# Kernel optimization log

Hardware: AMD Instinct MI355X
Metric: run time of the kernel (lower is better)

Reference implementation:

```python
import jax, jax.numpy as jnp
import numpy as np

B, T, D = 2, 4096, 512
H = 8
HD = D // H


def setup_inputs() -> dict:
    key = jax.random.key(0)
    ks = jax.random.split(key, 6)
    s = 0.02
    return {
        "token_embed": jax.random.normal(ks[0], (B, T, D), jnp.float32),
        "Wq": jax.random.normal(ks[1], (D, D), jnp.float32) * s,
        "Wk": jax.random.normal(ks[2], (D, D), jnp.float32) * s,
        "Wv": jax.random.normal(ks[3], (D, D), jnp.float32) * s,
        "Wo": jax.random.normal(ks[4], (D, D), jnp.float32) * s,
        "bo": jnp.zeros((D,), jnp.float32),
    }


def reference(token_embed, Wq, Wk, Wv, Wo, bo):
    b, t, d_in = token_embed.shape
    # QKV projections (Linear without bias): x @ W^T with W stored [d_out, d_in]
    q = jnp.einsum("btd,ed->bte", token_embed, Wq).reshape(b, t, H, HD).transpose(0, 2, 1, 3)
    k = jnp.einsum("btd,ed->bte", token_embed, Wk).reshape(b, t, H, HD).transpose(0, 2, 1, 3)
    v = jnp.einsum("btd,ed->bte", token_embed, Wv).reshape(b, t, H, HD).transpose(0, 2, 1, 3)
    # Scores [b, h, t, t] with causal mask applied before scaling (as in source)
    scores = jnp.einsum("bhqd,bhkd->bhqk", q, k)
    causal = jnp.tril(jnp.ones((t, t), bool))  # True = keep
    scores = jnp.where(causal, scores, -jnp.inf)
    attn = jax.nn.softmax(scores / jnp.sqrt(jnp.float32(HD)), axis=-1)
    # dropout p=0.0 -> identity
    ctx = jnp.einsum("bhqk,bhkd->bhqd", attn, v)
    ctx = ctx.transpose(0, 2, 1, 3).reshape(b, t, H * HD)
    return jnp.einsum("btd,ed->bte", ctx, Wo) + bo
```

## Files before the change

kernel.cpp:

```cpp
#include <hip/hip_runtime.h>

#define B_  2
#define T_  4096
#define D_  512
#define H_  8
#define HD_ 64
#define M_  (B_*T_)

typedef _Float16 h16;
typedef _Float16 v8h __attribute__((ext_vector_type(8)));
typedef float v4f __attribute__((ext_vector_type(4)));
typedef unsigned short us;

#define AS1 __attribute__((address_space(1)))
#define AS3 __attribute__((address_space(3)))

__device__ __forceinline__ float bf2f(us u){
  union { unsigned int i; float f; } v; v.i = ((unsigned int)u) << 16; return v.f;
}
__device__ __forceinline__ us f2bf(float f){
  union { float f; unsigned int u; } v; v.f = f;
  unsigned int r = v.u + 0x7FFFu + ((v.u >> 16) & 1u);
  return (us)(r >> 16);
}
__device__ __forceinline__ v4f zero4(){ v4f z; z[0]=0.f; z[1]=0.f; z[2]=0.f; z[3]=0.f; return z; }

__device__ __forceinline__ void glds16(const h16* g, h16* l){
  __builtin_amdgcn_global_load_lds((const AS1 int*)(const void*)g,
                                   (AS3 int*)(void*)l, 16, 0, 0);
}

__global__ __launch_bounds__(256) void conv_all(
    const void* __restrict__ x, const void* __restrict__ w0, const void* __restrict__ w1,
    const void* __restrict__ w2, const void* __restrict__ w3, const void* __restrict__ bo,
    h16* __restrict__ xb, h16* __restrict__ d0, h16* __restrict__ d1,
    h16* __restrict__ d2, h16* __restrict__ d3, float* __restrict__ bof)
{
  const int bid = blockIdx.x, tid = threadIdx.x;
  const void* src; int o0; int seg;
  h16* dst = nullptr;
  if (bid < 16384)      { src = x; o0 = bid * 256; dst = xb; seg = 0; }
  else if (bid < 20480) {
    const int wsel = (bid - 16384) >> 10;
    src = (wsel == 0) ? w0 : (wsel == 1) ? w1 : (wsel == 2) ? w2 : w3;
    dst = (wsel == 0) ? d0 : (wsel == 1) ? d1 : (wsel == 2) ? d2 : d3;
    o0 = ((bid - 16384) & 1023) * 256; seg = 0;
  } else                { src = bo; o0 = (bid - 20480) * 256; seg = 1; }

  __shared__ int sflag;
  if (tid == 0) sflag = 0;
  __syncthreads();
  const float probe = bf2f(((const us*)src)[o0 + tid]);
  if (!(fabsf(probe) < 1e4f)) atomicAdd(&sflag, 1);
  __syncthreads();
  const int isf32 = (sflag != 0);
  const int i = o0 + tid;
  const float v = isf32 ? ((const float*)src)[i] : bf2f(((const us*)src)[i]);
  if (seg) bof[i] = v;
  else     dst[i] = (h16)v;
}

__device__ __forceinline__ void stage4(const h16* __restrict__ A, const h16* __restrict__ W,
                                       int m0, int n0, int kk, h16* sA, h16* sB, int tid){
  const int colA = (tid & 3) << 3;
  const int rowT = tid >> 2;
#pragma unroll
  for (int rd = 0; rd < 2; rd++) {
    const int row = rd * 64 + rowT;
    const int f = rd * 2048 + tid * 8;
    glds16(A + (size_t)(m0 + row) * D_ + kk + colA, sA + f);
    glds16(W + (size_t)(n0 + row) * D_ + kk + colA, sB + f);
  }
}

__device__ __forceinline__ void gemm_core(const h16* __restrict__ A,
                                          const h16* __restrict__ W,
                                          int m0, int n0, h16* sA, h16* sB,
                                          v4f acc[4][4]) {
  const int tid = threadIdx.x;
  const int lane = tid & 63, wid = tid >> 6;
  const int r = lane & 15, q = lane >> 4;
#pragma unroll
  for (int i = 0; i < 4; i++)
#pragma unroll
    for (int j = 0; j < 4; j++) acc[i][j] = zero4();

  stage4(A, W, m0, n0, 0, sA, sB, tid);
#pragma unroll 1
  for (int kt = 0; kt < 16; kt++) {
    if (kt < 15) {
      const int nb = (kt + 1) & 1;
      stage4(A, W, m0, n0, (kt + 1) * 32, sA + nb * 4096, sB + nb * 4096, tid);
      asm volatile("s_waitcnt vmcnt(4)" ::: "memory");
    } else {
      asm volatile("s_waitcnt vmcnt(0)" ::: "memory");
    }
    asm volatile("s_barrier" ::: "memory");
    const h16* pA = sA + (kt & 1) * 4096 + ((wid & 1) * 64 + r) * 32 + q * 8;
    const h16* pB = sB + (kt & 1) * 4096 + ((wid >> 1) * 64 + r) * 32 + q * 8;
    v8h a[4], b[4];
#pragma unroll
    for (int i = 0; i < 4; i++) a[i] = *(const v8h*)(pA + i * 512);
#pragma unroll
    for (int j = 0; j < 4; j++) b[j] = *(const v8h*)(pB + j * 512);
#pragma unroll
    for (int i = 0; i < 4; i++)
#pragma unroll
      for (int j = 0; j < 4; j++)
        acc[i][j] = __builtin_amdgcn_mfma_f32_16x16x32_f16(a[i], b[j], acc[i][j], 0, 0, 0);
    asm volatile("s_barrier" ::: "memory");
  }
}

__global__ __launch_bounds__(256, 3) void gemm_qkv(
    const h16* __restrict__ X,
    const h16* __restrict__ Wq, const h16* __restrict__ Wk, const h16* __restrict__ Wv,
    h16* __restrict__ Qo, h16* __restrict__ Ko, h16* __restrict__ VTo)
{
  __shared__ h16 sA[2 * 4096], sB[2 * 4096];
  const h16* W = (blockIdx.z == 0) ? Wq : (blockIdx.z == 1 ? Wk : Wv);
  const int m0 = blockIdx.x * 128, n0 = blockIdx.y * 128;
  v4f acc[4][4];
  gemm_core(X, W, m0, n0, sA, sB, acc);
  const int lane = threadIdx.x & 63, wid = threadIdx.x >> 6;
  const int r = lane & 15, q = lane >> 4;
  const int wm = m0 + (wid & 1) * 64, wn = n0 + (wid >> 1) * 64;
  if (blockIdx.z == 2) {
#pragma unroll
    for (int i = 0; i < 4; i++)
#pragma unroll
      for (int j = 0; j < 4; j++)
#pragma unroll
        for (int rr = 0; rr < 4; rr++) {
          const int row = wm + i*16 + q*4 + rr;
          const int col = wn + j*16 + r;
          const int bb = row >> 12, tt = row & (T_ - 1);
          const int hh = col >> 6,  hd = col & 63;
          const int t6 = tt & 63;
          const int tperm = (tt & ~63) | (t6 & 3) | (((t6 >> 2) & 3) << 3)
                          | (((t6 >> 4) & 1) << 2) | (t6 & 32);
          VTo[((size_t)(((bb << 3) + hh) << 6) + hd) * T_ + tperm] = (h16)acc[i][j][rr];
        }
  } else {
    h16* Y = (blockIdx.z == 0) ? Qo : Ko;
    const float sc = (blockIdx.z == 0) ? 0.1803368801f : 1.0f;
#pragma unroll
    for (int i = 0; i < 4; i++)
#pragma unroll
      for (int j = 0; j < 4; j++)
#pragma unroll
        for (int rr = 0; rr < 4; rr++)
          Y[(size_t)(wm + i*16 + q*4 + rr) * D_ + wn + j*16 + r] = (h16)(acc[i][j][rr] * sc);
  }
}

__global__ __launch_bounds__(256, 3) void gemm_out(
    const h16* __restrict__ A, const h16* __restrict__ W,
    const float* __restrict__ bias, void* __restrict__ out, const void* __restrict__ xprobe)
{
  __shared__ h16 sA[2 * 4096], sB[2 * 4096];
  __shared__ int sflag;
  if (threadIdx.x == 0) sflag = 0;
  __syncthreads();
  const float probe = bf2f(((const us*)xprobe)[threadIdx.x]);
  if (!(fabsf(probe) < 1e4f)) atomicAdd(&sflag, 1);
  __syncthreads();
  const int flag = (sflag != 0);

  const int m0 = blockIdx.x * 128, n0 = blockIdx.y * 128;
  v4f acc[4][4];
  gemm_core(A, W, m0, n0, sA, sB, acc);
  const int lane = threadIdx.x & 63, wid = threadIdx.x >> 6;
  const int r = lane & 15, q = lane >> 4;
  const int wm = m0 + (wid & 1) * 64, wn = n0 + (wid >> 1) * 64;
#pragma unroll
  for (int i = 0; i < 4; i++)
#pragma unroll
    for (int j = 0; j < 4; j++)
#pragma unroll
      for (int rr = 0; rr < 4; rr++) {
        const int row = wm + i*16 + q*4 + rr;
        const int col = wn + j*16 + r;
        const float v = acc[i][j][rr] + bias[col];
        if (flag) ((float*)out)[(size_t)row * D_ + col] = v;
        else ((us*)out)[(size_t)row * D_ + col] = f2bf(v);
      }
}

__global__ __launch_bounds__(256, 4) void attn_kernel(
    const h16* __restrict__ Q, const h16* __restrict__ K,
    const h16* __restrict__ VT, h16* __restrict__ Ctx)
{
  const int h = blockIdx.x;
  const int pos = blockIdx.y + (blockIdx.z << 6);
  const int qc = 63 - (pos >> 1);
  const int b  = pos & 1;
  const int tid = threadIdx.x;
  const int wid = tid >> 6, lane = tid & 63;
  const int r = lane & 15, quad = lane >> 4;

  const size_t headoff = (size_t)b * T_ * D_ + (size_t)h * HD_;
  const h16* Qh  = Q + headoff;
  const h16* Kh  = K + headoff;
  const h16* VTh = VT + (size_t)(b * H_ + h) * HD_ * T_;
  h16* Ch = Ctx + headoff;

  __shared__ h16 sK[2][4096];
  __shared__ h16 sV[2][4096];

  const int qrow = qc * 64 + wid * 16;
  const int ntiles = qc + 1;

  const v8h aq0 = *(const v8h*)(Qh + (size_t)(qrow + r) * D_ + quad * 8);
  const v8h aq1 = *(const v8h*)(Qh + (size_t)(qrow + r) * D_ + 32 + quad * 8);

  v4f o[4];
#pragma unroll
  for (int j = 0; j < 4; j++) o[j] = zero4();
  float lsum = 0.f;

#pragma unroll
  for (int p = 0; p < 2; p++) {
    const int u = p * 256 + tid;
    const int row = u >> 3, j = u & 7, gj = j ^ (row & 7);
    glds16(Kh + (size_t)row * D_ + gj * 8, &sK[0][u * 8]);
  }
#pragma unroll
  for (int p = 0; p < 2; p++) {
    const int u = p * 256 + tid;
    const int row = u >> 3, j = u & 7, gj = j ^ (row & 7);
    glds16(VTh + (size_t)row * T_ + gj * 8, &sV[0][u * 8]);
  }

#pragma unroll 1
  for (int kt = 0; kt < ntiles; kt++) {
    const h16* sKc = sK[kt & 1];
    const h16* sVc = sV[kt & 1];
    if (kt + 1 < ntiles) {
      const int nb = (kt + 1) & 1;
      const int kb1 = (kt + 1) << 6;
#pragma unroll
      for (int p = 0; p < 2; p++) {
        const int u = p * 256 + tid;
        const int row = u >> 3, j = u & 7, gj = j ^ (row & 7);
        glds16(Kh + (size_t)(kb1 + row) * D_ + gj * 8, &sK[nb][u * 8]);
      }
#pragma unroll
      for (int p = 0; p < 2; p++) {
        const int u = p * 256 + tid;
        const int row = u >> 3, j = u & 7, gj = j ^ (row & 7);
        glds16(VTh + (size_t)row * T_ + kb1 + gj * 8, &sV[nb][u * 8]);
      }
      asm volatile("s_waitcnt vmcnt(4)" ::: "memory");
    } else {
      asm volatile("s_waitcnt vmcnt(0)" ::: "memory");
    }
    asm volatile("s_barrier" ::: "memory");

    const int kb = kt << 6;
    v8h ka[8], va[8];
#pragma unroll
    for (int kf = 0; kf < 4; kf++) {
      const int rowk = kf * 16 + r;
      const h16* base = sKc + rowk * 64;
      ka[2*kf]   = *(const v8h*)(base + ((quad     ^ (rowk & 7)) * 8));
      ka[2*kf+1] = *(const v8h*)(base + (((quad+4) ^ (rowk & 7)) * 8));
    }
#pragma unroll
    for (int j = 0; j < 4; j++) {
      const int rowv = j * 16 + r;
      const h16* base = sVc + rowv * 64;
      va[2*j]   = *(const v8h*)(base + ((quad     ^ (rowv & 7)) * 8));
      va[2*j+1] = *(const v8h*)(base + (((quad+4) ^ (rowv & 7)) * 8));
    }
    v4f s[4];
#pragma unroll
    for (int i = 0; i < 4; i++) {
      v4f t = zero4();
      t = __builtin_amdgcn_mfma_f32_16x16x32_f16(ka[2*i],   aq0, t, 0, 0, 0);
      t = __builtin_amdgcn_mfma_f32_16x16x32_f16(ka[2*i+1], aq1, t, 0, 0, 0);
      s[i] = t;
    }
    const bool maskt = (kt == ntiles - 1);
    v8h pa0, pa1;
#pragma unroll
    for (int i = 0; i < 4; i++) {
#pragma unroll
      for (int rr = 0; rr < 4; rr++) {
        float scv = s[i][rr];
        if (maskt) scv = (kb + i * 16 + quad * 4 + rr <= qrow + r) ? scv : -1e30f;
        const float e = exp2f(scv);
        lsum += e;
        if (i < 2) pa0[i * 4 + rr] = (h16)e;
        else       pa1[(i - 2) * 4 + rr] = (h16)e;
      }
    }
#pragma unroll
    for (int j = 0; j < 4; j++) {
      o[j] = __builtin_amdgcn_mfma_f32_16x16x32_f16(pa0, va[2*j],   o[j], 0, 0, 0);
      o[j] = __builtin_amdgcn_mfma_f32_16x16x32_f16(pa1, va[2*j+1], o[j], 0, 0, 0);
    }
    asm volatile("s_barrier" ::: "memory");
  }
  float l = lsum;
  l += __shfl_xor(l, 16, 64);
  l += __shfl_xor(l, 32, 64);
  const float inv = 1.0f / l;
  float invr[4];
#pragma unroll
  for (int rr = 0; rr < 4; rr++) invr[rr] = __shfl(inv, quad * 4 + rr, 16);
#pragma unroll
  for (int rr = 0; rr < 4; rr++) {
    const size_t row = (size_t)(qrow + quad * 4 + rr) * D_;
#pragma unroll
    for (int j = 0; j < 4; j++)
      Ch[row + j * 16 + r] = (h16)(o[j][rr] * invr[rr]);
  }
}

extern "C" void kernel_launch(void* const* d_in, const int* in_sizes, int n_in,
                              void* d_out, int out_size, void* d_ws, size_t ws_size,
                              hipStream_t stream) {
  char* ws = (char*)d_ws;
  h16* xb  = (h16*)(ws + 0);
  h16* qb  = (h16*)(ws + 8388608);
  h16* kb  = (h16*)(ws + 16777216);
  h16* vt  = (h16*)(ws + 25165824);
  h16* ctx = (h16*)(ws + 33554432);
  h16* wqb = (h16*)(ws + 41943040);
  h16* wkb = (h16*)(ws + 41943040 + 524288);
  h16* wvb = (h16*)(ws + 41943040 + 2 * 524288);
  h16* wob = (h16*)(ws + 41943040 + 3 * 524288);
  float* bof = (float*)(ws + 41943040 + 4 * 524288);

  conv_all<<<20482, 256, 0, stream>>>(d_in[0], d_in[1], d_in[2], d_in[3], d_in[4],
                                      d_in[5], xb, wqb, wkb, wvb, wob, bof);
  gemm_qkv<<<dim3(M_ / 128, D_ / 128, 3), 256, 0, stream>>>(xb, wqb, wkb, wvb, qb, kb, vt);
  attn_kernel<<<dim3(H_, 64, B_), 256, 0, stream>>>(qb, kb, vt, ctx);
  gemm_out<<<dim3(M_ / 128, D_ / 128, 1), 256, 0, stream>>>(ctx, wob, bof, d_out, d_in[0]);
}
```

Measured before the change: 196.8 us.

## Process two 64-row query groups per attention block to reuse K/V tiles

Each attention block now handles 128 query rows, as two 64-row groups, instead of 64, so every K/V tile loaded into shared memory serves both groups. This roughly halves global K/V traffic and barrier overhead per query row. Blocks are scheduled in a heavy/light interleaved order to balance causal work, and shared-memory pointer arithmetic is simplified with incrementing pointers. The grid is halved and launch bounds are relaxed to allow more registers, which risks lower occupancy and fewer blocks to fill the device.

```diff
diff --git a/kernel.cpp b/kernel.cpp
--- a/kernel.cpp
+++ b/kernel.cpp
@@ -187,14 +187,14 @@
       }
 }
 
-__global__ __launch_bounds__(256, 4) void attn_kernel(
+__global__ __launch_bounds__(256, 2) void attn_kernel(
     const h16* __restrict__ Q, const h16* __restrict__ K,
     const h16* __restrict__ VT, h16* __restrict__ Ctx)
 {
   const int h = blockIdx.x;
-  const int pos = blockIdx.y + (blockIdx.z << 6);
-  const int qc = 63 - (pos >> 1);
-  const int b  = pos & 1;
+  const int s = blockIdx.y + (blockIdx.z << 5);
+  const int qc = (s < 32) ? (31 - (s >> 1)) : ((s - 32) >> 1);
+  const int b  = s & 1;
   const int tid = threadIdx.x;
   const int wid = tid >> 6, lane = tid & 63;
   const int r = lane & 15, quad = lane >> 4;
@@ -208,29 +208,34 @@
   __shared__ h16 sK[2][4096];
   __shared__ h16 sV[2][4096];
 
-  const int qrow = qc * 64 + wid * 16;
-  const int ntiles = qc + 1;
-
-  const v8h aq0 = *(const v8h*)(Qh + (size_t)(qrow + r) * D_ + quad * 8);
-  const v8h aq1 = *(const v8h*)(Qh + (size_t)(qrow + r) * D_ + 32 + quad * 8);
-
-  v4f o[4];
-#pragma unroll
-  for (int j = 0; j < 4; j++) o[j] = zero4();
-  float lsum = 0.f;
-
-#pragma unroll
-  for (int p = 0; p < 2; p++) {
-    const int u = p * 256 + tid;
-    const int row = u >> 3, j = u & 7, gj = j ^ (row & 7);
-    glds16(Kh + (size_t)row * D_ + gj * 8, &sK[0][u * 8]);
-  }
-#pragma unroll
-  for (int p = 0; p < 2; p++) {
-    const int u = p * 256 + tid;
-    const int row = u >> 3, j = u & 7, gj = j ^ (row & 7);
-    glds16(VTh + (size_t)row * T_ + gj * 8, &sV[0][u * 8]);
-  }
+  const int qg0 = qc * 128 + wid * 16;
+  const int qg1 = qg0 + 64;
+  const int ntiles = 2 * qc + 2;
+  const int diag0 = 2 * qc, diag1 = 2 * qc + 1;
+
+  const v8h aq00 = *(const v8h*)(Qh + (size_t)(qg0 + r) * D_ + quad * 8);
+  const v8h aq01 = *(const v8h*)(Qh + (size_t)(qg0 + r) * D_ + 32 + quad * 8);
+  const v8h aq10 = *(const v8h*)(Qh + (size_t)(qg1 + r) * D_ + quad * 8);
+  const v8h aq11 = *(const v8h*)(Qh + (size_t)(qg1 + r) * D_ + 32 + quad * 8);
+
+  v4f o0[4], o1[4];
+#pragma unroll
+  for (int j = 0; j < 4; j++) { o0[j] = zero4(); o1[j] = zero4(); }
+  float lsum0 = 0.f, lsum1 = 0.f;
+
+  const int u0 = tid, u1 = tid + 256;
+  const int sr0 = u0 >> 3, sj0 = (u0 & 7) ^ (sr0 & 7);
+  const int sr1 = u1 >> 3, sj1 = (u1 & 7) ^ (sr1 & 7);
+  const h16* kp0 = Kh + (size_t)sr0 * D_ + sj0 * 8;
+  const h16* kp1 = Kh + (size_t)sr1 * D_ + sj1 * 8;
+  const h16* vp0 = VTh + (size_t)sr0 * T_ + sj0 * 8;
+  const h16* vp1 = VTh + (size_t)sr1 * T_ + sj1 * 8;
+
+  glds16(kp0, &sK[0][u0 * 8]);
+  glds16(kp1, &sK[0][u1 * 8]);
+  glds16(vp0, &sV[0][u0 * 8]);
+  glds16(vp1, &sV[0][u1 * 8]);
+  kp0 += 64 * D_; kp1 += 64 * D_; vp0 += 64; vp1 += 64;
 
 #pragma unroll 1
   for (int kt = 0; kt < ntiles; kt++) {
@@ -238,83 +243,89 @@
     const h16* sVc = sV[kt & 1];
     if (kt + 1 < ntiles) {
       const int nb = (kt + 1) & 1;
-      const int kb1 = (kt + 1) << 6;
-#pragma unroll
-      for (int p = 0; p < 2; p++) {
-        const int u = p * 256 + tid;
-        const int row = u >> 3, j = u & 7, gj = j ^ (row & 7);
-        glds16(Kh + (size_t)(kb1 + row) * D_ + gj * 8, &sK[nb][u * 8]);
-      }
-#pragma unroll
-      for (int p = 0; p < 2; p++) {
-        const int u = p * 256 + tid;
-        const int row = u >> 3, j = u & 7, gj = j ^ (row & 7);
-        glds16(VTh + (size_t)row * T_ + kb1 + gj * 8, &sV[nb][u * 8]);
-      }
+      glds16(kp0, &sK[nb][u0 * 8]);
+      glds16(kp1, &sK[nb][u1 * 8]);
+      glds16(vp0, &sV[nb][u0 * 8]);
+      glds16(vp1, &sV[nb][u1 * 8]);
+      kp0 += 64 * D_; kp1 += 64 * D_; vp0 += 64; vp1 += 64;
       asm volatile("s_waitcnt vmcnt(4)" ::: "memory");
     } else {
       asm volatile("s_waitcnt vmcnt(0)" ::: "memory");
     }
     asm volatile("s_barrier" ::: "memory");
 
-    const int kb = kt << 6;
     v8h ka[8], va[8];
 #pragma unroll
     for (int kf = 0; kf < 4; kf++) {
       const int rowk = kf * 16 + r;
       const h16* base = sKc + rowk * 64;
-      ka[2*kf]   = *(const v8h*)(base + ((quad     ^ (rowk & 7)) * 8));
-      ka[2*kf+1] = *(const v8h*)(base + (((quad+4) ^ (rowk & 7)) * 8));
+      ka[2*kf]   = *(const v8h*)(base + ((quad     ^ (r & 7)) * 8));
+      ka[2*kf+1] = *(const v8h*)(base + (((quad+4) ^ (r & 7)) * 8));
     }
 #pragma unroll
     for (int j = 0; j < 4; j++) {
       const int rowv = j * 16 + r;
       const h16* base = sVc + rowv * 64;
-      va[2*j]   = *(const v8h*)(base + ((quad     ^ (rowv & 7)) * 8));
-      va[2*j+1] = *(const v8h*)(base + (((quad+4) ^ (rowv & 7)) * 8));
-    }
-    v4f s[4];
-#pragma unroll
-    for (int i = 0; i < 4; i++) {
-      v4f t = zero4();
-      t = __builtin_amdgcn_mfma_f32_16x16x32_f16(ka[2*i],   aq0, t, 0, 0, 0);
-      t = __builtin_amdgcn_mfma_f32_16x16x32_f16(ka[2*i+1], aq1, t, 0, 0, 0);
-      s[i] = t;
-    }
-    const bool maskt = (kt == ntiles - 1);
-    v8h pa0, pa1;
-#pragma unroll
-    for (int i = 0; i < 4; i++) {
-#pragma unroll
-      for (int rr = 0; rr < 4; rr++) {
-        float scv = s[i][rr];
-        if (maskt) scv = (kb + i * 16 + quad * 4 + rr <= qrow + r) ? scv : -1e30f;
-        const float e = exp2f(scv);
-        lsum += e;
-        if (i < 2) pa0[i * 4 + rr] = (h16)e;
-        else       pa1[(i - 2) * 4 + rr] = (h16)e;
-      }
-    }
-#pragma unroll
-    for (int j = 0; j < 4; j++) {
-      o[j] = __builtin_amdgcn_mfma_f32_16x16x32_f16(pa0, va[2*j],   o[j], 0, 0, 0);
-      o[j] = __builtin_amdgcn_mfma_f32_16x16x32_f16(pa1, va[2*j+1], o[j], 0, 0, 0);
-    }
+      va[2*j]   = *(const v8h*)(base + ((quad     ^ (r & 7)) * 8));
+      va[2*j+1] = *(const v8h*)(base + (((quad+4) ^ (r & 7)) * 8));
+    }
+
+#define GROUP_COMPUTE(AQ0, AQ1, OARR, LSUM, DIAG)                              \
+    {                                                                          \
+      v4f s_[4];                                                               \
+      _Pragma("unroll")                                                        \
+      for (int i = 0; i < 4; i++) {                                            \
+        v4f t = zero4();                                                       \
+        t = __builtin_amdgcn_mfma_f32_16x16x32_f16(ka[2*i],   AQ0, t, 0,0,0);  \
+        t = __builtin_amdgcn_mfma_f32_16x16x32_f16(ka[2*i+1], AQ1, t, 0,0,0);  \
+        s_[i] = t;                                                             \
+      }                                                                        \
+      const bool dg_ = (kt == (DIAG));                                         \
+      v8h pa0, pa1;                                                            \
+      _Pragma("unroll")                                                        \
+      for (int i = 0; i < 4; i++) {                                            \
+        _Pragma("unroll")                                                      \
+        for (int rr = 0; rr < 4; rr++) {                                       \
+          float scv = s_[i][rr];                                               \
+          if (dg_) scv = (i*16 + quad*4 + rr <= wid*16 + r) ? scv : -1e30f;    \
+          const float e = exp2f(scv);                                          \
+          LSUM += e;                                                           \
+          if (i < 2) pa0[i*4+rr] = (h16)e; else pa1[(i-2)*4+rr] = (h16)e;      \
+        }                                                                      \
+      }                                                                        \
+      _Pragma("unroll")                                                        \
+      for (int j = 0; j < 4; j++) {                                            \
+        OARR[j] = __builtin_amdgcn_mfma_f32_16x16x32_f16(pa0, va[2*j],   OARR[j], 0,0,0); \
+        OARR[j] = __builtin_amdgcn_mfma_f32_16x16x32_f16(pa1, va[2*j+1], OARR[j], 0,0,0); \
+      }                                                                        \
+    }
+
+    if (kt <= diag0) GROUP_COMPUTE(aq00, aq01, o0, lsum0, diag0);
+    GROUP_COMPUTE(aq10, aq11, o1, lsum1, diag1);
+#undef GROUP_COMPUTE
+
     asm volatile("s_barrier" ::: "memory");
   }
-  float l = lsum;
-  l += __shfl_xor(l, 16, 64);
-  l += __shfl_xor(l, 32, 64);
-  const float inv = 1.0f / l;
-  float invr[4];
-#pragma unroll
-  for (int rr = 0; rr < 4; rr++) invr[rr] = __shfl(inv, quad * 4 + rr, 16);
-#pragma unroll
-  for (int rr = 0; rr < 4; rr++) {
-    const size_t row = (size_t)(qrow + quad * 4 + rr) * D_;
-#pragma unroll
-    for (int j = 0; j < 4; j++)
-      Ch[row + j * 16 + r] = (h16)(o[j][rr] * invr[rr]);
+
+#pragma unroll
+  for (int g = 0; g < 2; g++) {
+    const float lsum = g ? lsum1 : lsum0;
+    const int qg = g ? qg1 : qg0;
+    v4f* o = g ? o1 : o0;
+    float l = lsum;
+    l += __shfl_xor(l, 16, 64);
+    l += __shfl_xor(l, 32, 64);
+    const float inv = 1.0f / l;
+    float invr[4];
+#pragma unroll
+    for (int rr = 0; rr < 4; rr++) invr[rr] = __shfl(inv, quad * 4 + rr, 16);
+#pragma unroll
+    for (int rr = 0; rr < 4; rr++) {
+      const size_t row = (size_t)(qg + quad * 4 + rr) * D_;
+#pragma unroll
+      for (int j = 0; j < 4; j++)
+        Ch[row + j * 16 + r] = (h16)(o[j][rr] * invr[rr]);
+    }
   }
 }
 
@@ -336,6 +347,6 @@
   conv_all<<<20482, 256, 0, stream>>>(d_in[0], d_in[1], d_in[2], d_in[3], d_in[4],
                                       d_in[5], xb, wqb, wkb, wvb, wob, bof);
   gemm_qkv<<<dim3(M_ / 128, D_ / 128, 3), 256, 0, stream>>>(xb, wqb, wkb, wvb, qb, kb, vt);
-  attn_kernel<<<dim3(H_, 64, B_), 256, 0, stream>>>(qb, kb, vt, ctx);
+  attn_kernel<<<dim3(H_, 32, B_), 256, 0, stream>>>(qb, kb, vt, ctx);
   gemm_out<<<dim3(M_ / 128, D_ / 128, 1), 256, 0, stream>>>(ctx, wob, bof, d_out, d_in[0]);
 }
```

After: 213.9 us. +8.7%, slower.
